# Performance work log

Hardware: AMD Instinct MI355X
Metric: run time of the kernel (lower is better)

## Reference

```python
import jax, jax.numpy as jnp
import numpy as np

D = 256; NH = 8; NL = 4; NP = 4; DFF = 2048; HD = D // NH
SHAPES = [(64, 64), (32, 32), (16, 16), (8, 8)]
B = 2; LEN = sum(h * w for h, w in SHAPES)


def setup_inputs() -> dict:
    key = jax.random.key(0)
    ks = jax.random.split(key, 12)
    def w(k, shape, s=0.02):
        return jax.random.normal(k, shape, jnp.float32) * s
    starts = np.cumsum([0] + [h * w for h, w in SHAPES[:-1]])
    return {
        "src": jax.random.normal(ks[0], (B, LEN, D), jnp.float32),
        "pos": jax.random.normal(ks[1], (B, LEN, D), jnp.float32) * 0.1,
        "spatial_shapes": jnp.array(SHAPES, dtype=jnp.int32),
        "level_start_index": jnp.array(starts, dtype=jnp.int32),
        "w_value": w(ks[2], (D, D)), "b_value": jnp.zeros((D,), jnp.float32),
        "w_off": w(ks[3], (D, NH * NL * NP * 2)), "b_off": w(ks[4], (NH * NL * NP * 2,), 0.1),
        "w_attn": w(ks[5], (D, NH * NL * NP)), "b_attn": jnp.zeros((NH * NL * NP,), jnp.float32),
        "w_out": w(ks[6], (D, D)), "b_out": jnp.zeros((D,), jnp.float32),
        "w1": w(ks[7], (D, DFF)), "b1": jnp.zeros((DFF,), jnp.float32),
        "w2": w(ks[8], (DFF, D)), "b2": jnp.zeros((D,), jnp.float32),
        "g1": jnp.ones((D,), jnp.float32), "be1": jnp.zeros((D,), jnp.float32),
        "g2": jnp.ones((D,), jnp.float32), "be2": jnp.zeros((D,), jnp.float32),
    }


def _layer_norm(x, g, b):
    mu = jnp.mean(x, -1, keepdims=True)
    v = jnp.var(x, -1, keepdims=True)
    return (x - mu) * jax.lax.rsqrt(v + 1e-5) * g + b


def _reference_points(shapes):
    # torch.linspace(0.5, H-0.5, H)/H == (arange(H)+0.5)/H
    refs = []
    for H, W in shapes:
        ry = (jnp.arange(H, dtype=jnp.float32) + 0.5) / H
        rx = (jnp.arange(W, dtype=jnp.float32) + 0.5) / W
        yy, xx = jnp.meshgrid(ry, rx, indexing='ij')
        refs.append(jnp.stack([xx.ravel(), yy.ravel()], -1))
    return jnp.concatenate(refs, 0)  # (Len, 2) as (x, y)


def _ms_deform_sample(value, loc, shapes):
    # value: (B, Len, NH, HD); loc: (B, Lq, NH, NL, NP, 2) normalized [0,1]
    # Replicates torch grid_sample(bilinear, padding='zeros', align_corners=False).
    Bn, Lq = loc.shape[0], loc.shape[1]
    P = loc.shape[4]
    start = 0
    outs = []
    for lvl, (H, W) in enumerate(shapes):
        v = value[:, start:start + H * W].transpose(0, 2, 1, 3)  # (B, NH, HW, HD)
        start += H * W
        l = loc[:, :, :, lvl]                      # (B, Lq, NH, P, 2)
        x = l[..., 0] * W - 0.5
        y = l[..., 1] * H - 0.5
        x0 = jnp.floor(x); y0 = jnp.floor(y)
        dx = x - x0; dy = y - y0
        x0i = x0.astype(jnp.int32); y0i = y0.astype(jnp.int32)
        acc = None
        for xi, yi, wgt in ((x0i, y0i, (1 - dx) * (1 - dy)),
                            (x0i + 1, y0i, dx * (1 - dy)),
                            (x0i, y0i + 1, (1 - dx) * dy),
                            (x0i + 1, y0i + 1, dx * dy)):
            valid = ((xi >= 0) & (xi < W) & (yi >= 0) & (yi < H)).astype(value.dtype)
            idx = jnp.clip(yi, 0, H - 1) * W + jnp.clip(xi, 0, W - 1)  # (B, Lq, NH, P)
            idx = idx.transpose(0, 2, 1, 3).reshape(Bn, NH, Lq * P)
            g = jnp.take_along_axis(v, idx[..., None], axis=2).reshape(Bn, NH, Lq, P, HD)
            w = (wgt * valid).transpose(0, 2, 1, 3)[..., None]  # (B, NH, Lq, P, 1)
            acc = g * w if acc is None else acc + g * w
        outs.append(acc)  # (B, NH, Lq, P, HD)
    return jnp.stack(outs, 3)  # (B, NH, Lq, NL, NP, HD)


def _forward(src, pos, w_value, b_value, w_off, b_off, w_attn, b_attn,
             w_out, b_out, w1, b1, w2, b2, g1, be1, g2, be2, shapes):
    Bn, Lq, _ = src.shape
    q = src + pos  # with_pos_embed
    value = (src @ w_value + b_value).reshape(Bn, Lq, NH, HD)
    off = (q @ w_off + b_off).reshape(Bn, Lq, NH, NL, NP, 2)
    attn = jax.nn.softmax((q @ w_attn + b_attn).reshape(Bn, Lq, NH, NL * NP), -1)
    attn = attn.reshape(Bn, Lq, NH, NL, NP)
    ref = _reference_points(shapes)  # (Len, 2)
    normalizer = jnp.array([[w_, h_] for h_, w_ in shapes], jnp.float32)  # (NL, 2) = (W, H)
    loc = ref[None, :, None, None, None, :] + off / normalizer[None, None, None, :, None, :]
    sampled = _ms_deform_sample(value, loc, shapes)  # (B, NH, Lq, NL, NP, HD)
    out = jnp.einsum('bqhlp,bhqlpd->bqhd', attn, sampled).reshape(Bn, Lq, D)
    out = out @ w_out + b_out
    x = _layer_norm(src + out, g1, be1)           # residual + norm1
    ff = jax.nn.relu(x @ w1 + b1) @ w2 + b2       # FFN (dropout=0)
    return _layer_norm(x + ff, g2, be2)           # residual + norm2


def reference(src, pos, spatial_shapes, level_start_index, w_value, b_value,
              w_off, b_off, w_attn, b_attn, w_out, b_out, w1, b1, w2, b2,
              g1, be1, g2, be2):
    shapes = [tuple(int(v) for v in s) for s in np.asarray(spatial_shapes)]
    return _forward(src, pos, w_value, b_value, w_off, b_off, w_attn, b_attn,
                    w_out, b_out, w1, b1, w2, b2, g1, be1, g2, be2, shapes)
```

## Files before the change

### kernel.cpp

```cpp
#include <hip/hip_runtime.h>
#include <math.h>

#define D 256
#define NH 8
#define NL 4
#define NP 4
#define DFF 2048
#define HD 32
#define BB 2
#define LEN 5440
#define MROWS (BB * LEN)

typedef __attribute__((ext_vector_type(8))) short short8;
typedef __attribute__((ext_vector_type(4))) float f32x4;
typedef unsigned int uint32;

__device__ __forceinline__ unsigned short f2bf(float f) {
    uint32 u = __float_as_uint(f);
    u += 0x7FFF + ((u >> 16) & 1);
    return (unsigned short)(u >> 16);
}
__device__ __forceinline__ float bf2f(unsigned short h) {
    return __uint_as_float(((uint32)h) << 16);
}
__device__ __forceinline__ uint32 pack2(float a, float b) {
    return (uint32)f2bf(a) | ((uint32)f2bf(b) << 16);
}

__device__ __forceinline__ void swz85(int b, int ncols, int& row, int& col) {
    const int gsz = ncols << 3;
    const int full = 10 * gsz;
    if (b < full) {
        const int g = b / gsz, idx = b - g * gsz;
        row = (g << 3) + (idx & 7);
        col = idx >> 3;
    } else {
        const int idx = b - full;
        row = 80 + idx % 5;
        col = idx / 5;
    }
}

__global__ void prep(const float* __restrict__ w_value, const float* __restrict__ w_off,
                     const float* __restrict__ w_attn, const float* __restrict__ w_out,
                     const float* __restrict__ w1, const float* __restrict__ w2,
                     const float* __restrict__ b_value, const float* __restrict__ b_off,
                     const float* __restrict__ b_attn,
                     unsigned short* __restrict__ wqvT, unsigned short* __restrict__ woT,
                     unsigned short* __restrict__ w1T, unsigned short* __restrict__ w2T,
                     float* __restrict__ bqv) {
    const int blk = blockIdx.x;
    if (blk >= 1248) {
        for (int i = threadIdx.x; i < 640; i += 256)
            bqv[i] = (i < 256) ? b_value[i] : (i < 512 ? b_off[i - 256] : b_attn[i - 512]);
        return;
    }
    const float* W; unsigned short* WT; int K, N, tid;
    if (blk < 64)       { W = w_value; WT = wqvT;             K = 256;  N = 256;  tid = blk; }
    else if (blk < 128) { W = w_off;   WT = wqvT + 256 * 256; K = 256;  N = 256;  tid = blk - 64; }
    else if (blk < 160) { W = w_attn;  WT = wqvT + 512 * 256; K = 256;  N = 128;  tid = blk - 128; }
    else if (blk < 224) { W = w_out;   WT = woT;              K = 256;  N = 256;  tid = blk - 160; }
    else if (blk < 736) { W = w1;      WT = w1T;              K = 256;  N = 2048; tid = blk - 224; }
    else                { W = w2;      WT = w2T;              K = 2048; N = 256;  tid = blk - 736; }
    const int ntx = N >> 5;
    const int nb = (tid % ntx) * 32, kb = (tid / ntx) * 32;

    __shared__ float tile[32][33];
    const int tx = threadIdx.x & 31, ty = threadIdx.x >> 5;
#pragma unroll
    for (int i = 0; i < 32; i += 8)
        tile[ty + i][tx] = W[(size_t)(kb + ty + i) * N + nb + tx];
    __syncthreads();
#pragma unroll
    for (int i = 0; i < 32; i += 8)
        WT[(size_t)(nb + ty + i) * K + kb + tx] = f2bf(tile[tx][ty + i]);
}

__global__ __launch_bounds__(256) void ffn1_gemm(
        const unsigned short* __restrict__ A,
        const unsigned short* __restrict__ BT, const float* __restrict__ bias,
        unsigned short* __restrict__ Cv, int N, int K, int lda, int ldb) {
    __shared__ unsigned short Ash[128][40];
    __shared__ unsigned short Bsh[128][40];

    int rowt, colt;
    swz85(blockIdx.x, N >> 7, rowt, colt);
    const int row0 = rowt * 128, col0 = colt * 128;

    const int t = threadIdx.x;
    const int wave = t >> 6, lane = t & 63;
    const int wr = wave >> 1, wc = wave & 1;
    const int lrow = lane & 15, quad = lane >> 4;
    const int srow = t >> 1;
    const int cb = (t & 1) * 16;

    const unsigned short* ap = A + (size_t)(row0 + srow) * lda + cb;
    const unsigned short* bp = BT + (size_t)(col0 + srow) * ldb + cb;

    f32x4 acc[4][4];
#pragma unroll
    for (int i = 0; i < 4; i++)
#pragma unroll
        for (int j = 0; j < 4; j++) acc[i][j] = (f32x4){0.f, 0.f, 0.f, 0.f};

    uint4 ra0 = *(const uint4*)(ap + 0), ra1 = *(const uint4*)(ap + 8);
    uint4 rb0 = *(const uint4*)(bp + 0), rb1 = *(const uint4*)(bp + 8);

    for (int kb = 0; kb < K; kb += 32) {
        __syncthreads();
        *(uint4*)&Ash[srow][cb + 0] = ra0;
        *(uint4*)&Ash[srow][cb + 8] = ra1;
        *(uint4*)&Bsh[srow][cb + 0] = rb0;
        *(uint4*)&Bsh[srow][cb + 8] = rb1;
        __syncthreads();
        if (kb + 32 < K) {
            ra0 = *(const uint4*)(ap + kb + 32 + 0);
            ra1 = *(const uint4*)(ap + kb + 32 + 8);
            rb0 = *(const uint4*)(bp + kb + 32 + 0);
            rb1 = *(const uint4*)(bp + kb + 32 + 8);
        }

        short8 af[4], bfr[4];
#pragma unroll
        for (int mt = 0; mt < 4; mt++)
            af[mt] = *(const short8*)&Ash[wr * 64 + mt * 16 + lrow][quad * 8];
#pragma unroll
        for (int nt = 0; nt < 4; nt++)
            bfr[nt] = *(const short8*)&Bsh[wc * 64 + nt * 16 + lrow][quad * 8];
#pragma unroll
        for (int mt = 0; mt < 4; mt++)
#pragma unroll
            for (int nt = 0; nt < 4; nt++)
                acc[mt][nt] = __builtin_amdgcn_mfma_f32_16x16x32_bf16(
                    af[mt], bfr[nt], acc[mt][nt], 0, 0, 0);
    }

#pragma unroll
    for (int nt = 0; nt < 4; nt++) {
        const int col = col0 + wc * 64 + nt * 16 + lrow;
        const float bv = bias[col];
#pragma unroll
        for (int mt = 0; mt < 4; mt++) {
            f32x4 a = acc[mt][nt];
#pragma unroll
            for (int r = 0; r < 4; r++) {
                const int row = row0 + wr * 64 + mt * 16 + quad * 4 + r;
                Cv[(size_t)row * N + col] = f2bf(fmaxf(a[r] + bv, 0.f));
            }
        }
    }
}

template <int NZ>
__global__ __launch_bounds__(256) void splitk_gemm(
        const unsigned short* __restrict__ A, const unsigned short* __restrict__ BT,
        unsigned short* __restrict__ part, int KC, int lda, int ldb) {
    __shared__ unsigned short Ash[128][40];
    __shared__ unsigned short Bsh[128][40];

    int rowt, cc;
    swz85(blockIdx.x, 2 * NZ, rowt, cc);
    const int row0 = rowt * 128;
    const int col0 = (cc & 1) * 128;
    const int z = cc >> 1;
    const int koff = z * KC;
    unsigned short* __restrict__ C = part + (size_t)z * MROWS * 256;

    const int t = threadIdx.x;
    const int wave = t >> 6, lane = t & 63;
    const int wr = wave >> 1, wc = wave & 1;
    const int lrow = lane & 15, quad = lane >> 4;
    const int srow = t >> 1;
    const int cb = (t & 1) * 16;

    const unsigned short* ap = A + (size_t)(row0 + srow) * lda + koff + cb;
    const unsigned short* bp = BT + (size_t)(col0 + srow) * ldb + koff + cb;

    f32x4 acc[4][4];
#pragma unroll
    for (int i = 0; i < 4; i++)
#pragma unroll
        for (int j = 0; j < 4; j++) acc[i][j] = (f32x4){0.f, 0.f, 0.f, 0.f};

    uint4 ra0 = *(const uint4*)(ap + 0), ra1 = *(const uint4*)(ap + 8);
    uint4 rb0 = *(const uint4*)(bp + 0), rb1 = *(const uint4*)(bp + 8);

    for (int kb = 0; kb < KC; kb += 32) {
        __syncthreads();
        *(uint4*)&Ash[srow][cb + 0] = ra0;
        *(uint4*)&Ash[srow][cb + 8] = ra1;
        *(uint4*)&Bsh[srow][cb + 0] = rb0;
        *(uint4*)&Bsh[srow][cb + 8] = rb1;
        __syncthreads();
        if (kb + 32 < KC) {
            ra0 = *(const uint4*)(ap + kb + 32 + 0);
            ra1 = *(const uint4*)(ap + kb + 32 + 8);
            rb0 = *(const uint4*)(bp + kb + 32 + 0);
            rb1 = *(const uint4*)(bp + kb + 32 + 8);
        }

        short8 af[4], bfr[4];
#pragma unroll
        for (int mt = 0; mt < 4; mt++)
            af[mt] = *(const short8*)&Ash[wr * 64 + mt * 16 + lrow][quad * 8];
#pragma unroll
        for (int nt = 0; nt < 4; nt++)
            bfr[nt] = *(const short8*)&Bsh[wc * 64 + nt * 16 + lrow][quad * 8];
#pragma unroll
        for (int mt = 0; mt < 4; mt++)
#pragma unroll
            for (int nt = 0; nt < 4; nt++)
                acc[mt][nt] = __builtin_amdgcn_mfma_f32_16x16x32_bf16(
                    af[mt], bfr[nt], acc[mt][nt], 0, 0, 0);
    }

#pragma unroll
    for (int nt = 0; nt < 4; nt++) {
        const int col = col0 + wc * 64 + nt * 16 + lrow;
#pragma unroll
        for (int mt = 0; mt < 4; mt++) {
            f32x4 a = acc[mt][nt];
#pragma unroll
            for (int r = 0; r < 4; r++) {
                const int row = row0 + wr * 64 + mt * 16 + quad * 4 + r;
                C[(size_t)row * 256 + col] = f2bf(a[r]);
            }
        }
    }
}

__global__ __launch_bounds__(256) void gemm_ln(
        const unsigned short* __restrict__ A, const unsigned short* __restrict__ BT,
        const float* __restrict__ bias, const float* __restrict__ rsd,
        const float* __restrict__ g, const float* __restrict__ be,
        unsigned short* __restrict__ out16, int K) {
    __shared__ __align__(16) unsigned short Ash[32][40];
    __shared__ __align__(16) unsigned short Bsh[256][40];
    __shared__ float red1[4][32], red2[4][32];

    const int row0 = blockIdx.x * 32;
    const int t = threadIdx.x;
    const int wave = t >> 6, lane = t & 63;
    const int lrow = lane & 15, quad = lane >> 4;

    const int ar = t >> 3, ac = (t & 7) * 4;
    const unsigned short* ap = A + (size_t)(row0 + ar) * K + ac;
    const int br = t >> 1, cb = (t & 1) * 16;
    const unsigned short* bp0 = BT + (size_t)br * K + cb;
    const unsigned short* bp1 = BT + (size_t)(128 + br) * K + cb;

    f32x4 acc[2][4];
#pragma unroll
    for (int i = 0; i < 2; i++)
#pragma unroll
        for (int j = 0; j < 4; j++) acc[i][j] = (f32x4){0.f, 0.f, 0.f, 0.f};

    uint2 ra = *(const uint2*)ap;
    uint4 rb00 = *(const uint4*)(bp0 + 0), rb01 = *(const uint4*)(bp0 + 8);
    uint4 rb10 = *(const uint4*)(bp1 + 0), rb11 = *(const uint4*)(bp1 + 8);

    for (int kb = 0; kb < K; kb += 32) {
        __syncthreads();
        *(uint2*)&Ash[ar][ac] = ra;
        *(uint4*)&Bsh[br][cb + 0] = rb00;
        *(uint4*)&Bsh[br][cb + 8] = rb01;
        *(uint4*)&Bsh[128 + br][cb + 0] = rb10;
        *(uint4*)&Bsh[128 + br][cb + 8] = rb11;
        __syncthreads();
        if (kb + 32 < K) {
            ra   = *(const uint2*)(ap + kb + 32);
            rb00 = *(const uint4*)(bp0 + kb + 32 + 0);
            rb01 = *(const uint4*)(bp0 + kb + 32 + 8);
            rb10 = *(const uint4*)(bp1 + kb + 32 + 0);
            rb11 = *(const uint4*)(bp1 + kb + 32 + 8);
        }

        short8 af[2], bfr[4];
#pragma unroll
        for (int mt = 0; mt < 2; mt++)
            af[mt] = *(const short8*)&Ash[mt * 16 + lrow][quad * 8];
#pragma unroll
        for (int nt = 0; nt < 4; nt++)
            bfr[nt] = *(const short8*)&Bsh[wave * 64 + nt * 16 + lrow][quad * 8];
#pragma unroll
        for (int mt = 0; mt < 2; mt++)
#pragma unroll
            for (int nt = 0; nt < 4; nt++)
                acc[mt][nt] = __builtin_amdgcn_mfma_f32_16x16x32_bf16(
                    af[mt], bfr[nt], acc[mt][nt], 0, 0, 0);
    }

    float gv[4], bev[4], bv[4];
#pragma unroll
    for (int nt = 0; nt < 4; nt++) {
        const int col = wave * 64 + nt * 16 + lrow;
        bv[nt] = bias[col];
        gv[nt] = g[col];
        bev[nt] = be[col];
    }

    float v[2][4][4];
#pragma unroll
    for (int mt = 0; mt < 2; mt++)
#pragma unroll
        for (int r = 0; r < 4; r++) {
            const int row = row0 + mt * 16 + quad * 4 + r;
#pragma unroll
            for (int nt = 0; nt < 4; nt++) {
                const int col = wave * 64 + nt * 16 + lrow;
                v[mt][nt][r] = acc[mt][nt][r] + bv[nt] + rsd[(size_t)row * 256 + col];
            }
        }

#pragma unroll
    for (int mt = 0; mt < 2; mt++)
#pragma unroll
        for (int r = 0; r < 4; r++) {
            float s1 = v[mt][0][r] + v[mt][1][r] + v[mt][2][r] + v[mt][3][r];
            float s2 = v[mt][0][r] * v[mt][0][r] + v[mt][1][r] * v[mt][1][r] +
                       v[mt][2][r] * v[mt][2][r] + v[mt][3][r] * v[mt][3][r];
#pragma unroll
            for (int o = 1; o < 16; o <<= 1) {
                s1 += __shfl_xor(s1, o, 16);
                s2 += __shfl_xor(s2, o, 16);
            }
            if (lrow == 0) {
                const int rr = mt * 16 + quad * 4 + r;
                red1[wave][rr] = s1;
                red2[wave][rr] = s2;
            }
        }
    __syncthreads();

#pragma unroll
    for (int mt = 0; mt < 2; mt++)
#pragma unroll
        for (int r = 0; r < 4; r++) {
            const int rr = mt * 16 + quad * 4 + r;
            const float su = red1[0][rr] + red1[1][rr] + red1[2][rr] + red1[3][rr];
            const float sq = red2[0][rr] + red2[1][rr] + red2[2][rr] + red2[3][rr];
            const float mean = su * (1.0f / 256.0f);
            const float var = fmaxf(sq * (1.0f / 256.0f) - mean * mean, 0.f);
            const float rstd = rsqrtf(var + 1e-5f);
            const size_t rowoff = (size_t)(row0 + rr) * 256;
#pragma unroll
            for (int nt = 0; nt < 4; nt++) {
                const int col = wave * 64 + nt * 16 + lrow;
                const float o = (v[mt][nt][r] - mean) * rstd * gv[nt] + bev[nt];
                out16[rowoff + col] = f2bf(o);
            }
        }
}

__global__ __launch_bounds__(256) void qv_gemm(
        const float* __restrict__ src, const float* __restrict__ pos,
        const unsigned short* __restrict__ BT, const float* __restrict__ bias,
        unsigned short* __restrict__ val, unsigned short* __restrict__ qout16) {
    __shared__ unsigned short Ash[128][40];
    __shared__ unsigned short Bsh[128][40];

    int rowt, colt;
    swz85(blockIdx.x, 5, rowt, colt);
    const int row0 = rowt * 128, col0 = colt * 128;
    const bool addp = (col0 >= 256);

    const int t = threadIdx.x;
    const int wave = t >> 6, lane = t & 63;
    const int wr = wave >> 1, wc = wave & 1;
    const int lrow = lane & 15, quad = lane >> 4;
    const int srow = t >> 1;
    const int cb = (t & 1) * 16;

    const float* ap = src + (size_t)(row0 + srow) * 256 + cb;
    const float* pp = pos + (size_t)(row0 + srow) * 256 + cb;
    const unsigned short* bp = BT + (size_t)(col0 + srow) * 256 + cb;

    f32x4 acc[4][4];
#pragma unroll
    for (int i = 0; i < 4; i++)
#pragma unroll
        for (int j = 0; j < 4; j++) acc[i][j] = (f32x4){0.f, 0.f, 0.f, 0.f};

    float4 fa[4]; float4 fp[4]; uint4 rb0, rb1;
#pragma unroll
    for (int j = 0; j < 4; j++) fa[j] = *(const float4*)(ap + 4 * j);
    if (addp) {
#pragma unroll
        for (int j = 0; j < 4; j++) fp[j] = *(const float4*)(pp + 4 * j);
    }
    rb0 = *(const uint4*)(bp + 0);
    rb1 = *(const uint4*)(bp + 8);

    for (int kb = 0; kb < 256; kb += 32) {
        __syncthreads();
        {
            float4 f0 = fa[0], f1 = fa[1], f2 = fa[2], f3 = fa[3];
            if (addp) {
                f0.x += fp[0].x; f0.y += fp[0].y; f0.z += fp[0].z; f0.w += fp[0].w;
                f1.x += fp[1].x; f1.y += fp[1].y; f1.z += fp[1].z; f1.w += fp[1].w;
                f2.x += fp[2].x; f2.y += fp[2].y; f2.z += fp[2].z; f2.w += fp[2].w;
                f3.x += fp[3].x; f3.y += fp[3].y; f3.z += fp[3].z; f3.w += fp[3].w;
            }
            uint4 u0 = make_uint4(pack2(f0.x, f0.y), pack2(f0.z, f0.w),
                                  pack2(f1.x, f1.y), pack2(f1.z, f1.w));
            uint4 u1 = make_uint4(pack2(f2.x, f2.y), pack2(f2.z, f2.w),
                                  pack2(f3.x, f3.y), pack2(f3.z, f3.w));
            *(uint4*)&Ash[srow][cb + 0] = u0;
            *(uint4*)&Ash[srow][cb + 8] = u1;
            *(uint4*)&Bsh[srow][cb + 0] = rb0;
            *(uint4*)&Bsh[srow][cb + 8] = rb1;
        }
        __syncthreads();
        if (kb + 32 < 256) {
#pragma unroll
            for (int j = 0; j < 4; j++) fa[j] = *(const float4*)(ap + kb + 32 + 4 * j);
            if (addp) {
#pragma unroll
                for (int j = 0; j < 4; j++) fp[j] = *(const float4*)(pp + kb + 32 + 4 * j);
            }
            rb0 = *(const uint4*)(bp + kb + 32 + 0);
            rb1 = *(const uint4*)(bp + kb + 32 + 8);
        }

        short8 af[4], bfr[4];
#pragma unroll
        for (int mt = 0; mt < 4; mt++)
            af[mt] = *(const short8*)&Ash[wr * 64 + mt * 16 + lrow][quad * 8];
#pragma unroll
        for (int nt = 0; nt < 4; nt++)
            bfr[nt] = *(const short8*)&Bsh[wc * 64 + nt * 16 + lrow][quad * 8];
#pragma unroll
        for (int mt = 0; mt < 4; mt++)
#pragma unroll
            for (int nt = 0; nt < 4; nt++)
                acc[mt][nt] = __builtin_amdgcn_mfma_f32_16x16x32_bf16(
                    af[mt], bfr[nt], acc[mt][nt], 0, 0, 0);
    }

#pragma unroll
    for (int nt = 0; nt < 4; nt++) {
        const int col = col0 + wc * 64 + nt * 16 + lrow;
        const float bv = bias[col];
#pragma unroll
        for (int mt = 0; mt < 4; mt++) {
            f32x4 a = acc[mt][nt];
#pragma unroll
            for (int r = 0; r < 4; r++) {
                const int row = row0 + wr * 64 + mt * 16 + quad * 4 + r;
                float v = a[r] + bv;
                if (col < 256)
                    val[(size_t)row * 256 + col] = f2bf(v);
                else
                    qout16[(size_t)row * 384 + (col - 256)] = f2bf(v);
            }
        }
    }
}

__global__ void sampler(const unsigned short* __restrict__ val,
                        const unsigned short* __restrict__ qout16,
                        unsigned short* __restrict__ out) {
    __shared__ __align__(16) int   sIdx[2][128][4];
    __shared__ __align__(16) float sW[2][128][4];
    const int t = threadIdx.x;
    const int sub = t >> 7;
    const int tt = t & 127;
    const int bq = blockIdx.x * 2 + sub;
    const int b = bq / LEN, q = bq % LEN;

    {
        const int h = tt >> 4, p = tt & 15;
        const int l = p >> 2;

        float refx, refy;
        if (q < 4096) {
            int rq = q >> 6, cq = q & 63;
            refx = (cq + 0.5f) * (1.0f / 64.0f);
            refy = (rq + 0.5f) * (1.0f / 64.0f);
        } else if (q < 5120) {
            int qq = q - 4096;
            int rq = qq >> 5, cq = qq & 31;
            refx = (cq + 0.5f) * (1.0f / 32.0f);
            refy = (rq + 0.5f) * (1.0f / 32.0f);
        } else if (q < 5376) {
            int qq = q - 5120;
            int rq = qq >> 4, cq = qq & 15;
            refx = (cq + 0.5f) * (1.0f / 16.0f);
            refy = (rq + 0.5f) * (1.0f / 16.0f);
        } else {
            int qq = q - 5376;
            int rq = qq >> 3, cq = qq & 7;
            refx = (cq + 0.5f) * (1.0f / 8.0f);
            refy = (rq + 0.5f) * (1.0f / 8.0f);
        }

        float lv = bf2f(qout16[(size_t)bq * 384 + 256 + tt]);
        float mx = lv;
#pragma unroll
        for (int o = 1; o < 16; o <<= 1) mx = fmaxf(mx, __shfl_xor(mx, o, 16));
        float e = expf(lv - mx);
        float s = e;
#pragma unroll
        for (int o = 1; o < 16; o <<= 1) s += __shfl_xor(s, o, 16);
        const float aw = e / s;

        const uint32 opair = *(const uint32*)&qout16[(size_t)bq * 384 + h * 32 + p * 2];
        const float ox = bf2f((unsigned short)opair);
        const float oy = bf2f((unsigned short)(opair >> 16));

        const int LST[4] = {0, 4096, 5120, 5376};
        const int WW = 64 >> l;
        const float rw = 1.0f / (float)WW;

        float x = (refx + ox * rw) * (float)WW - 0.5f;
        float y = (refy + oy * rw) * (float)WW - 0.5f;
        float x0f = floorf(x), y0f = floorf(y);
        float dx = x - x0f, dy = y - y0f;
        int x0 = (int)x0f, y0 = (int)y0f;

        const int base = (b * LEN + LST[l]) * 256 + h * 32;
        int xs[2] = {x0, x0 + 1}, ys[2] = {y0, y0 + 1};
        float wx[2] = {1.f - dx, dx}, wy[2] = {1.f - dy, dy};
        int ic[4]; float wc4[4];
#pragma unroll
        for (int cy = 0; cy < 2; cy++)
#pragma unroll
            for (int cx = 0; cx < 2; cx++) {
                int xi = xs[cx], yi = ys[cy];
                bool vld = (xi >= 0) && (xi < WW) && (yi >= 0) && (yi < WW);
                int xc = min(max(xi, 0), WW - 1);
                int yc = min(max(yi, 0), WW - 1);
                ic[cy * 2 + cx] = base + (yc * WW + xc) * 256;
                wc4[cy * 2 + cx] = vld ? wx[cx] * wy[cy] * aw : 0.f;
            }
        *(int4*)&sIdx[sub][tt][0] = make_int4(ic[0], ic[1], ic[2], ic[3]);
        *(float4*)&sW[sub][tt][0] = make_float4(wc4[0], wc4[1], wc4[2], wc4[3]);
    }
    __syncthreads();

    const int h = tt >> 4, dp = tt & 15;
    const unsigned short* vald = val + 2 * dp;
    float acc0 = 0.f, acc1 = 0.f;
#pragma unroll 4
    for (int p = 0; p < 16; p++) {
        const int r = h * 16 + p;
        int4 iv = *(const int4*)&sIdx[sub][r][0];
        float4 wv = *(const float4*)&sW[sub][r][0];
        uint32 u0 = *(const uint32*)(vald + iv.x);
        uint32 u1 = *(const uint32*)(vald + iv.y);
        uint32 u2 = *(const uint32*)(vald + iv.z);
        uint32 u3 = *(const uint32*)(vald + iv.w);
        acc0 += bf2f((unsigned short)u0) * wv.x + bf2f((unsigned short)u1) * wv.y +
                bf2f((unsigned short)u2) * wv.z + bf2f((unsigned short)u3) * wv.w;
        acc1 += bf2f((unsigned short)(u0 >> 16)) * wv.x + bf2f((unsigned short)(u1 >> 16)) * wv.y +
                bf2f((unsigned short)(u2 >> 16)) * wv.z + bf2f((unsigned short)(u3 >> 16)) * wv.w;
    }
    *(uint32*)&out[(size_t)bq * D + h * HD + 2 * dp] = pack2(acc0, acc1);
}

__global__ void add_ln4(const unsigned short* __restrict__ part16,
                        const float* __restrict__ bias,
                        const unsigned short* __restrict__ rsd16,
                        const float* __restrict__ g, const float* __restrict__ be,
                        float* __restrict__ out) {
    const int wave = threadIdx.x >> 6, lane = threadIdx.x & 63;
    const int row = blockIdx.x * 4 + wave;
    const int c0 = lane * 4;
    const size_t i = (size_t)row * 256 + c0;

    float v[4];
    {
        ushort4 r = *(const ushort4*)&rsd16[i];
        float4 bv = *(const float4*)&bias[c0];
        v[0] = bf2f(r.x) + bv.x; v[1] = bf2f(r.y) + bv.y;
        v[2] = bf2f(r.z) + bv.z; v[3] = bf2f(r.w) + bv.w;
    }
#pragma unroll
    for (int z = 0; z < 4; z++) {
        ushort4 p = *(const ushort4*)&part16[(size_t)z * MROWS * 256 + i];
        v[0] += bf2f(p.x); v[1] += bf2f(p.y); v[2] += bf2f(p.z); v[3] += bf2f(p.w);
    }
    float s1 = v[0] + v[1] + v[2] + v[3];
    float s2 = v[0] * v[0] + v[1] * v[1] + v[2] * v[2] + v[3] * v[3];
#pragma unroll
    for (int o = 32; o > 0; o >>= 1) {
        s1 += __shfl_xor(s1, o, 64);
        s2 += __shfl_xor(s2, o, 64);
    }
    const float mean = s1 * (1.0f / 256.0f);
    const float var = fmaxf(s2 * (1.0f / 256.0f) - mean * mean, 0.f);
    const float rstd = rsqrtf(var + 1e-5f);

    float4 gv = *(const float4*)&g[c0];
    float4 bev = *(const float4*)&be[c0];
    float4 o4;
    o4.x = (v[0] - mean) * rstd * gv.x + bev.x;
    o4.y = (v[1] - mean) * rstd * gv.y + bev.y;
    o4.z = (v[2] - mean) * rstd * gv.z + bev.z;
    o4.w = (v[3] - mean) * rstd * gv.w + bev.w;
    *(float4*)&out[i] = o4;
}

extern "C" void kernel_launch(void* const* d_in, const int* in_sizes, int n_in,
                              void* d_out, int out_size, void* d_ws, size_t ws_size,
                              hipStream_t stream) {
    const float* src     = (const float*)d_in[0];
    const float* pos     = (const float*)d_in[1];
    const float* w_value = (const float*)d_in[4];
    const float* b_value = (const float*)d_in[5];
    const float* w_off   = (const float*)d_in[6];
    const float* b_off   = (const float*)d_in[7];
    const float* w_attn  = (const float*)d_in[8];
    const float* b_attn  = (const float*)d_in[9];
    const float* w_out   = (const float*)d_in[10];
    const float* b_out   = (const float*)d_in[11];
    const float* w1      = (const float*)d_in[12];
    const float* b1      = (const float*)d_in[13];
    const float* w2      = (const float*)d_in[14];
    const float* b2      = (const float*)d_in[15];
    const float* g1      = (const float*)d_in[16];
    const float* be1     = (const float*)d_in[17];
    const float* g2      = (const float*)d_in[18];
    const float* be2     = (const float*)d_in[19];
    float* out = (float*)d_out;

    size_t off = 0;
    auto alloc = [&](size_t bytes) -> char* {
        char* p = (char*)d_ws + off;
        off += (bytes + 255) & ~(size_t)255;
        return p;
    };
    unsigned short* wqvT = (unsigned short*)alloc((size_t)640 * 256 * 2);
    unsigned short* woT  = (unsigned short*)alloc(256 * 256 * 2);
    unsigned short* w1T  = (unsigned short*)alloc((size_t)2048 * 256 * 2);
    unsigned short* w2T  = (unsigned short*)alloc((size_t)256 * 2048 * 2);
    float* bqv           = (float*)alloc(640 * 4);

    unsigned short* qout = (unsigned short*)alloc((size_t)MROWS * 384 * 2);
    unsigned short* val  = (unsigned short*)alloc((size_t)MROWS * 256 * 2);
    unsigned short* attn = (unsigned short*)alloc((size_t)MROWS * 256 * 2);
    unsigned short* hb   = (unsigned short*)alloc((size_t)MROWS * 2048 * 2);
    unsigned short* xb16 = (unsigned short*)alloc((size_t)MROWS * 256 * 2);
    unsigned short* part = (unsigned short*)alloc((size_t)4 * MROWS * 256 * 2);

    prep<<<1249, 256, 0, stream>>>(w_value, w_off, w_attn, w_out, w1, w2,
                                   b_value, b_off, b_attn, wqvT, woT, w1T, w2T, bqv);

    qv_gemm<<<425, 256, 0, stream>>>(src, pos, wqvT, bqv, val, qout);
    sampler<<<MROWS / 2, 256, 0, stream>>>(val, qout, attn);
    gemm_ln<<<340, 256, 0, stream>>>(attn, woT, b_out, src, g1, be1, xb16, 256);

    ffn1_gemm<<<1360, 256, 0, stream>>>(xb16, w1T, b1, hb, 2048, 256, 256, 256);
    splitk_gemm<4><<<680, 256, 0, stream>>>(hb, w2T, part, 512, 2048, 2048);
    add_ln4<<<MROWS / 4, 256, 0, stream>>>(part, b2, xb16, g2, be2, out);
}
```

Measured before the change: 205.6 us.

## Double-buffer shared-memory tiles in GEMM kernels to halve barriers per k-step

Converts the ffn1, split-K and qv GEMM kernels from single-buffered LDS tiles with two barriers per k-iteration to ping-pong double buffers with one barrier per iteration. The next tile is written into the alternate buffer while MFMAs read the current one, and the global prefetch is pushed two stages ahead. The cost is doubled LDS use per block (about 40KB), which may reduce occupancy, plus longer register lifetimes for the staged data.

```diff
diff --git a/kernel.cpp b/kernel.cpp
--- a/kernel.cpp
+++ b/kernel.cpp
@@ -80,8 +80,8 @@
         const unsigned short* __restrict__ A,
         const unsigned short* __restrict__ BT, const float* __restrict__ bias,
         unsigned short* __restrict__ Cv, int N, int K, int lda, int ldb) {
-    __shared__ unsigned short Ash[128][40];
-    __shared__ unsigned short Bsh[128][40];
+    __shared__ unsigned short Ash[2][128][40];
+    __shared__ unsigned short Bsh[2][128][40];
 
     int rowt, colt;
     swz85(blockIdx.x, N >> 7, rowt, colt);
@@ -105,28 +105,39 @@
 
     uint4 ra0 = *(const uint4*)(ap + 0), ra1 = *(const uint4*)(ap + 8);
     uint4 rb0 = *(const uint4*)(bp + 0), rb1 = *(const uint4*)(bp + 8);
-
-    for (int kb = 0; kb < K; kb += 32) {
-        __syncthreads();
-        *(uint4*)&Ash[srow][cb + 0] = ra0;
-        *(uint4*)&Ash[srow][cb + 8] = ra1;
-        *(uint4*)&Bsh[srow][cb + 0] = rb0;
-        *(uint4*)&Bsh[srow][cb + 8] = rb1;
+    *(uint4*)&Ash[0][srow][cb + 0] = ra0;
+    *(uint4*)&Ash[0][srow][cb + 8] = ra1;
+    *(uint4*)&Bsh[0][srow][cb + 0] = rb0;
+    *(uint4*)&Bsh[0][srow][cb + 8] = rb1;
+    if (32 < K) {
+        ra0 = *(const uint4*)(ap + 32); ra1 = *(const uint4*)(ap + 40);
+        rb0 = *(const uint4*)(bp + 32); rb1 = *(const uint4*)(bp + 40);
+    }
+
+    int i = 0;
+    for (int kb = 0; kb < K; kb += 32, ++i) {
         __syncthreads();
         if (kb + 32 < K) {
-            ra0 = *(const uint4*)(ap + kb + 32 + 0);
-            ra1 = *(const uint4*)(ap + kb + 32 + 8);
-            rb0 = *(const uint4*)(bp + kb + 32 + 0);
-            rb1 = *(const uint4*)(bp + kb + 32 + 8);
-        }
-
+            const int nb = (i + 1) & 1;
+            *(uint4*)&Ash[nb][srow][cb + 0] = ra0;
+            *(uint4*)&Ash[nb][srow][cb + 8] = ra1;
+            *(uint4*)&Bsh[nb][srow][cb + 0] = rb0;
+            *(uint4*)&Bsh[nb][srow][cb + 8] = rb1;
+            if (kb + 64 < K) {
+                ra0 = *(const uint4*)(ap + kb + 64 + 0);
+                ra1 = *(const uint4*)(ap + kb + 64 + 8);
+                rb0 = *(const uint4*)(bp + kb + 64 + 0);
+                rb1 = *(const uint4*)(bp + kb + 64 + 8);
+            }
+        }
+        const int cf = i & 1;
         short8 af[4], bfr[4];
 #pragma unroll
         for (int mt = 0; mt < 4; mt++)
-            af[mt] = *(const short8*)&Ash[wr * 64 + mt * 16 + lrow][quad * 8];
+            af[mt] = *(const short8*)&Ash[cf][wr * 64 + mt * 16 + lrow][quad * 8];
 #pragma unroll
         for (int nt = 0; nt < 4; nt++)
-            bfr[nt] = *(const short8*)&Bsh[wc * 64 + nt * 16 + lrow][quad * 8];
+            bfr[nt] = *(const short8*)&Bsh[cf][wc * 64 + nt * 16 + lrow][quad * 8];
 #pragma unroll
         for (int mt = 0; mt < 4; mt++)
 #pragma unroll
@@ -155,8 +166,8 @@
 __global__ __launch_bounds__(256) void splitk_gemm(
         const unsigned short* __restrict__ A, const unsigned short* __restrict__ BT,
         unsigned short* __restrict__ part, int KC, int lda, int ldb) {
-    __shared__ unsigned short Ash[128][40];
-    __shared__ unsigned short Bsh[128][40];
+    __shared__ unsigned short Ash[2][128][40];
+    __shared__ unsigned short Bsh[2][128][40];
 
     int rowt, cc;
     swz85(blockIdx.x, 2 * NZ, rowt, cc);
@@ -184,28 +195,39 @@
 
     uint4 ra0 = *(const uint4*)(ap + 0), ra1 = *(const uint4*)(ap + 8);
     uint4 rb0 = *(const uint4*)(bp + 0), rb1 = *(const uint4*)(bp + 8);
-
-    for (int kb = 0; kb < KC; kb += 32) {
-        __syncthreads();
-        *(uint4*)&Ash[srow][cb + 0] = ra0;
-        *(uint4*)&Ash[srow][cb + 8] = ra1;
-        *(uint4*)&Bsh[srow][cb + 0] = rb0;
-        *(uint4*)&Bsh[srow][cb + 8] = rb1;
+    *(uint4*)&Ash[0][srow][cb + 0] = ra0;
+    *(uint4*)&Ash[0][srow][cb + 8] = ra1;
+    *(uint4*)&Bsh[0][srow][cb + 0] = rb0;
+    *(uint4*)&Bsh[0][srow][cb + 8] = rb1;
+    if (32 < KC) {
+        ra0 = *(const uint4*)(ap + 32); ra1 = *(const uint4*)(ap + 40);
+        rb0 = *(const uint4*)(bp + 32); rb1 = *(const uint4*)(bp + 40);
+    }
+
+    int i = 0;
+    for (int kb = 0; kb < KC; kb += 32, ++i) {
         __syncthreads();
         if (kb + 32 < KC) {
-            ra0 = *(const uint4*)(ap + kb + 32 + 0);
-            ra1 = *(const uint4*)(ap + kb + 32 + 8);
-            rb0 = *(const uint4*)(bp + kb + 32 + 0);
-            rb1 = *(const uint4*)(bp + kb + 32 + 8);
-        }
-
+            const int nb = (i + 1) & 1;
+            *(uint4*)&Ash[nb][srow][cb + 0] = ra0;
+            *(uint4*)&Ash[nb][srow][cb + 8] = ra1;
+            *(uint4*)&Bsh[nb][srow][cb + 0] = rb0;
+            *(uint4*)&Bsh[nb][srow][cb + 8] = rb1;
+            if (kb + 64 < KC) {
+                ra0 = *(const uint4*)(ap + kb + 64 + 0);
+                ra1 = *(const uint4*)(ap + kb + 64 + 8);
+                rb0 = *(const uint4*)(bp + kb + 64 + 0);
+                rb1 = *(const uint4*)(bp + kb + 64 + 8);
+            }
+        }
+        const int cf = i & 1;
         short8 af[4], bfr[4];
 #pragma unroll
         for (int mt = 0; mt < 4; mt++)
-            af[mt] = *(const short8*)&Ash[wr * 64 + mt * 16 + lrow][quad * 8];
+            af[mt] = *(const short8*)&Ash[cf][wr * 64 + mt * 16 + lrow][quad * 8];
 #pragma unroll
         for (int nt = 0; nt < 4; nt++)
-            bfr[nt] = *(const short8*)&Bsh[wc * 64 + nt * 16 + lrow][quad * 8];
+            bfr[nt] = *(const short8*)&Bsh[cf][wc * 64 + nt * 16 + lrow][quad * 8];
 #pragma unroll
         for (int mt = 0; mt < 4; mt++)
 #pragma unroll
@@ -356,8 +378,8 @@
         const float* __restrict__ src, const float* __restrict__ pos,
         const unsigned short* __restrict__ BT, const float* __restrict__ bias,
         unsigned short* __restrict__ val, unsigned short* __restrict__ qout16) {
-    __shared__ unsigned short Ash[128][40];
-    __shared__ unsigned short Bsh[128][40];
+    __shared__ unsigned short Ash[2][128][40];
+    __shared__ unsigned short Bsh[2][128][40];
 
     int rowt, colt;
     swz85(blockIdx.x, 5, rowt, colt);
@@ -382,53 +404,53 @@
         for (int j = 0; j < 4; j++) acc[i][j] = (f32x4){0.f, 0.f, 0.f, 0.f};
 
     float4 fa[4]; float4 fp[4]; uint4 rb0, rb1;
-#pragma unroll
-    for (int j = 0; j < 4; j++) fa[j] = *(const float4*)(ap + 4 * j);
-    if (addp) {
-#pragma unroll
-        for (int j = 0; j < 4; j++) fp[j] = *(const float4*)(pp + 4 * j);
-    }
-    rb0 = *(const uint4*)(bp + 0);
-    rb1 = *(const uint4*)(bp + 8);
-
-    for (int kb = 0; kb < 256; kb += 32) {
-        __syncthreads();
-        {
-            float4 f0 = fa[0], f1 = fa[1], f2 = fa[2], f3 = fa[3];
-            if (addp) {
-                f0.x += fp[0].x; f0.y += fp[0].y; f0.z += fp[0].z; f0.w += fp[0].w;
-                f1.x += fp[1].x; f1.y += fp[1].y; f1.z += fp[1].z; f1.w += fp[1].w;
-                f2.x += fp[2].x; f2.y += fp[2].y; f2.z += fp[2].z; f2.w += fp[2].w;
-                f3.x += fp[3].x; f3.y += fp[3].y; f3.z += fp[3].z; f3.w += fp[3].w;
-            }
-            uint4 u0 = make_uint4(pack2(f0.x, f0.y), pack2(f0.z, f0.w),
-                                  pack2(f1.x, f1.y), pack2(f1.z, f1.w));
-            uint4 u1 = make_uint4(pack2(f2.x, f2.y), pack2(f2.z, f2.w),
-                                  pack2(f3.x, f3.y), pack2(f3.z, f3.w));
-            *(uint4*)&Ash[srow][cb + 0] = u0;
-            *(uint4*)&Ash[srow][cb + 8] = u1;
-            *(uint4*)&Bsh[srow][cb + 0] = rb0;
-            *(uint4*)&Bsh[srow][cb + 8] = rb1;
-        }
+    auto packA = [&](int buf) {
+        float4 f0 = fa[0], f1 = fa[1], f2 = fa[2], f3 = fa[3];
+        if (addp) {
+            f0.x += fp[0].x; f0.y += fp[0].y; f0.z += fp[0].z; f0.w += fp[0].w;
+            f1.x += fp[1].x; f1.y += fp[1].y; f1.z += fp[1].z; f1.w += fp[1].w;
+            f2.x += fp[2].x; f2.y += fp[2].y; f2.z += fp[2].z; f2.w += fp[2].w;
+            f3.x += fp[3].x; f3.y += fp[3].y; f3.z += fp[3].z; f3.w += fp[3].w;
+        }
+        uint4 u0 = make_uint4(pack2(f0.x, f0.y), pack2(f0.z, f0.w),
+                              pack2(f1.x, f1.y), pack2(f1.z, f1.w));
+        uint4 u1 = make_uint4(pack2(f2.x, f2.y), pack2(f2.z, f2.w),
+                              pack2(f3.x, f3.y), pack2(f3.z, f3.w));
+        *(uint4*)&Ash[buf][srow][cb + 0] = u0;
+        *(uint4*)&Ash[buf][srow][cb + 8] = u1;
+        *(uint4*)&Bsh[buf][srow][cb + 0] = rb0;
+        *(uint4*)&Bsh[buf][srow][cb + 8] = rb1;
+    };
+    auto loadA = [&](int kb) {
+#pragma unroll
+        for (int j = 0; j < 4; j++) fa[j] = *(const float4*)(ap + kb + 4 * j);
+        if (addp) {
+#pragma unroll
+            for (int j = 0; j < 4; j++) fp[j] = *(const float4*)(pp + kb + 4 * j);
+        }
+        rb0 = *(const uint4*)(bp + kb + 0);
+        rb1 = *(const uint4*)(bp + kb + 8);
+    };
+
+    loadA(0);
+    packA(0);
+    loadA(32);
+
+    int i = 0;
+    for (int kb = 0; kb < 256; kb += 32, ++i) {
         __syncthreads();
         if (kb + 32 < 256) {
-#pragma unroll
-            for (int j = 0; j < 4; j++) fa[j] = *(const float4*)(ap + kb + 32 + 4 * j);
-            if (addp) {
-#pragma unroll
-                for (int j = 0; j < 4; j++) fp[j] = *(const float4*)(pp + kb + 32 + 4 * j);
-            }
-            rb0 = *(const uint4*)(bp + kb + 32 + 0);
-            rb1 = *(const uint4*)(bp + kb + 32 + 8);
-        }
-
+            packA((i + 1) & 1);
+            if (kb + 64 < 256) loadA(kb + 64);
+        }
+        const int cf = i & 1;
         short8 af[4], bfr[4];
 #pragma unroll
         for (int mt = 0; mt < 4; mt++)
-            af[mt] = *(const short8*)&Ash[wr * 64 + mt * 16 + lrow][quad * 8];
+            af[mt] = *(const short8*)&Ash[cf][wr * 64 + mt * 16 + lrow][quad * 8];
 #pragma unroll
         for (int nt = 0; nt < 4; nt++)
-            bfr[nt] = *(const short8*)&Bsh[wc * 64 + nt * 16 + lrow][quad * 8];
+            bfr[nt] = *(const short8*)&Bsh[cf][wc * 64 + nt * 16 + lrow][quad * 8];
 #pragma unroll
         for (int mt = 0; mt < 4; mt++)
 #pragma unroll
```

After: 203.3 us. No clear change (-1.1%).
